# Performance work log

Measured on AMD Instinct MI355X. Metric: run time of the kernel, lower is better.

## Reference

```python
import jax, jax.numpy as jnp
import numpy as np

T = 262144        # sequence_length
K = 512           # num_basis
DEGREE = 3
EPS = 1e-6


def setup_inputs() -> dict:
    # Deterministic buffers, matching the torch module's __init__ exactly.
    t = jnp.linspace(-1.0, 1.0, T, dtype=jnp.float32)
    num_knots = K + DEGREE + 1
    inner = jnp.linspace(-1.0, 1.0, num_knots - 2 * DEGREE, dtype=jnp.float32)
    knots = jnp.concatenate([
        jnp.full((DEGREE,), -1.0, dtype=jnp.float32),
        inner,
        jnp.full((DEGREE,), 1.0, dtype=jnp.float32),
    ])
    return {"t": t, "knots": knots}


def _bspline(t, kv):
    n0 = K + DEGREE  # number of degree-0 basis functions
    tc = t[:, None]  # [T, 1]
    # degree-0: indicator of [kv[i], kv[i+1]) ; last interval is closed.
    cond1 = tc >= kv[None, :n0]
    cond2 = tc < kv[None, 1:n0 + 1]
    last_closed = tc <= kv[None, n0:n0 + 1]
    cond2 = jnp.concatenate([cond2[:, :-1], last_closed], axis=1)
    bases = (cond1 & cond2).astype(t.dtype)  # [T, K+DEGREE]
    # Cox-de Boor recursion, vectorized over knot index i.
    for d in range(1, DEGREE + 1):
        n = K + DEGREE - d
        den1 = kv[d:d + n] - kv[:n]            # [n]
        den2 = kv[d + 1:d + n + 1] - kv[1:n + 1]
        c1 = jnp.where(den1 >= EPS, (tc - kv[None, :n]) / jnp.where(den1 >= EPS, den1, 1.0), 0.0)
        c2 = jnp.where(den2 >= EPS, (kv[None, d + 1:d + n + 1] - tc) / jnp.where(den2 >= EPS, den2, 1.0), 0.0)
        bases = c1 * bases[:, :n] + c2 * bases[:, 1:n + 1]
    return bases  # [T, K]


def reference(t, knots):
    return _bspline(t, knots)
```

## Files before the change

### kernel.cpp

```cpp
#include <hip/hip_runtime.h>


namespace {
constexpr int K_N  = 512;
constexpr int NKN  = 516;
constexpr int DEG  = 3;
constexpr float EPSF = 1e-6f;
constexpr int ROWS = 16;
constexpr int BLK  = 256;
}

__global__ __launch_bounds__(BLK)
void bspline_basis_kernel(const float* __restrict__ t_arr,
                          const float* __restrict__ knots,
                          float* __restrict__ out)
{
    __shared__ float kv[NKN];

    const int tid = threadIdx.x;
    for (int i = tid; i < NKN; i += BLK) kv[i] = knots[i];

    const int row_base = blockIdx.x * ROWS;
    float4* out4 = reinterpret_cast<float4*>(out + (size_t)row_base * K_N);

    __syncthreads();

    int   j0 = -1;
    float N0 = 0.f, N1 = 0.f, N2 = 0.f, N3 = 0.f;
    if (tid < ROWS) {
        const float t = t_arr[row_base + tid];
        if (t < kv[K_N]) {
            int lo = DEG, hi = K_N - 1;
            while (lo < hi) {
                const int mid = (lo + hi + 1) >> 1;
                if (t >= kv[mid]) lo = mid; else hi = mid - 1;
            }
            const int s = lo;
            float N[4] = {1.f, 0.f, 0.f, 0.f};
            #pragma unroll
            for (int d = 1; d <= DEG; ++d) {
                float nn[4];
                #pragma unroll
                for (int k = 0; k <= d; ++k) {
                    const int j = s - d + k;
                    const float left  = (k >= 1)     ? N[k - 1] : 0.f;
                    const float right = (k <= d - 1) ? N[k]     : 0.f;
                    const float den1 = kv[j + d]     - kv[j];
                    const float den2 = kv[j + d + 1] - kv[j + 1];
                    const float c1 = (den1 >= EPSF) ? (t - kv[j]) / den1 : 0.f;
                    const float c2 = (den2 >= EPSF) ? (kv[j + d + 1] - t) / den2 : 0.f;
                    nn[k] = c1 * left + c2 * right;
                }
                #pragma unroll
                for (int k = 0; k <= d; ++k) N[k] = nn[k];
            }
            j0 = s - DEG;
            N0 = N[0]; N1 = N[1]; N2 = N[2]; N3 = N[3];
        }
    }

    const float4 z = make_float4(0.f, 0.f, 0.f, 0.f);
    constexpr int TOTAL_F4 = ROWS * (K_N / 4);
    #pragma unroll
    for (int it = 0; it < TOTAL_F4 / BLK; ++it)
        out4[it * BLK + tid] = z;

    __syncthreads();

    if (tid < ROWS && j0 >= 0) {
        float* p = out + (size_t)(row_base + tid) * K_N + j0;
        p[0] = N0; p[1] = N1; p[2] = N2; p[3] = N3;
    }
}

extern "C" void kernel_launch(void* const* d_in, const int* in_sizes, int n_in,
                              void* d_out, int out_size, void* d_ws, size_t ws_size,
                              hipStream_t stream) {
    const float* t_arr = (const float*)d_in[0];
    const float* knots = (const float*)d_in[1];
    float* out = (float*)d_out;
    const int n_rows = in_sizes[0];
    dim3 grid(n_rows / ROWS);
    hipLaunchKernelGGL(bspline_basis_kernel, grid, dim3(BLK), 0, stream,
                       t_arr, knots, out);
}
```

Measured before the change: 538.7 us.

## Split into grid-stride zero-fill kernel and window-write kernel with eight lanes per row

Splits the work into a grid-stride zero-fill kernel over the whole output and a second kernel where eight lanes per row each compute the basis and write float4 chunks covering the nonzero window. Moving the zeroing out of the per-row blocks is meant to make the dominant 512 MB write a dense streaming store. The cost is rewriting the window region a second time from another launch, plus eight-fold redundant binary search and recursion per row.

```diff
diff --git a/kernel.cpp b/kernel.cpp
--- a/kernel.cpp
+++ b/kernel.cpp
@@ -6,70 +6,87 @@
 constexpr int NKN  = 516;
 constexpr int DEG  = 3;
 constexpr float EPSF = 1e-6f;
-constexpr int ROWS = 16;
 constexpr int BLK  = 256;
+constexpr int ROWS_PER_BLK_B = 32;
 }
 
 __global__ __launch_bounds__(BLK)
-void bspline_basis_kernel(const float* __restrict__ t_arr,
-                          const float* __restrict__ knots,
-                          float* __restrict__ out)
+void zero_fill_kernel(float4* __restrict__ out4, int n4)
+{
+    const int stride = gridDim.x * BLK;
+    const float4 z = make_float4(0.f, 0.f, 0.f, 0.f);
+    for (int i = blockIdx.x * BLK + threadIdx.x; i < n4; i += stride)
+        out4[i] = z;
+}
+
+__global__ __launch_bounds__(BLK)
+void window_kernel(const float* __restrict__ t_arr,
+                   const float* __restrict__ knots,
+                   float* __restrict__ out)
 {
     __shared__ float kv[NKN];
-
     const int tid = threadIdx.x;
     for (int i = tid; i < NKN; i += BLK) kv[i] = knots[i];
-
-    const int row_base = blockIdx.x * ROWS;
-    float4* out4 = reinterpret_cast<float4*>(out + (size_t)row_base * K_N);
-
     __syncthreads();
 
-    int   j0 = -1;
-    float N0 = 0.f, N1 = 0.f, N2 = 0.f, N3 = 0.f;
-    if (tid < ROWS) {
-        const float t = t_arr[row_base + tid];
-        if (t < kv[K_N]) {
-            int lo = DEG, hi = K_N - 1;
-            while (lo < hi) {
-                const int mid = (lo + hi + 1) >> 1;
-                if (t >= kv[mid]) lo = mid; else hi = mid - 1;
-            }
-            const int s = lo;
-            float N[4] = {1.f, 0.f, 0.f, 0.f};
-            #pragma unroll
-            for (int d = 1; d <= DEG; ++d) {
-                float nn[4];
-                #pragma unroll
-                for (int k = 0; k <= d; ++k) {
-                    const int j = s - d + k;
-                    const float left  = (k >= 1)     ? N[k - 1] : 0.f;
-                    const float right = (k <= d - 1) ? N[k]     : 0.f;
-                    const float den1 = kv[j + d]     - kv[j];
-                    const float den2 = kv[j + d + 1] - kv[j + 1];
-                    const float c1 = (den1 >= EPSF) ? (t - kv[j]) / den1 : 0.f;
-                    const float c2 = (den2 >= EPSF) ? (kv[j + d + 1] - t) / den2 : 0.f;
-                    nn[k] = c1 * left + c2 * right;
-                }
-                #pragma unroll
-                for (int k = 0; k <= d; ++k) N[k] = nn[k];
-            }
-            j0 = s - DEG;
-            N0 = N[0]; N1 = N[1]; N2 = N[2]; N3 = N[3];
+    const int q   = tid & 7;
+    const int row = blockIdx.x * ROWS_PER_BLK_B + (tid >> 3);
+    const float t = t_arr[row];
+
+    if (t >= kv[K_N]) return;
+
+    int lo = DEG, hi = K_N - 1;
+    while (lo < hi) {
+        const int mid = (lo + hi + 1) >> 1;
+        if (t >= kv[mid]) lo = mid; else hi = mid - 1;
+    }
+    const int s = lo;
+
+    float N[4] = {1.f, 0.f, 0.f, 0.f};
+    #pragma unroll
+    for (int d = 1; d <= DEG; ++d) {
+        float nn[4];
+        #pragma unroll
+        for (int k = 0; k <= d; ++k) {
+            const int j = s - d + k;
+            const float left  = (k >= 1)     ? N[k - 1] : 0.f;
+            const float right = (k <= d - 1) ? N[k]     : 0.f;
+            const float den1 = kv[j + d]     - kv[j];
+            const float den2 = kv[j + d + 1] - kv[j + 1];
+            const float c1 = (den1 >= EPSF) ? (t - kv[j]) / den1 : 0.f;
+            const float c2 = (den2 >= EPSF) ? (kv[j + d + 1] - t) / den2 : 0.f;
+            nn[k] = c1 * left + c2 * right;
         }
+        #pragma unroll
+        for (int k = 0; k <= d; ++k) N[k] = nn[k];
     }
+    const int j0 = s - DEG;
 
-    const float4 z = make_float4(0.f, 0.f, 0.f, 0.f);
-    constexpr int TOTAL_F4 = ROWS * (K_N / 4);
-    #pragma unroll
-    for (int it = 0; it < TOTAL_F4 / BLK; ++it)
-        out4[it * BLK + tid] = z;
+    float4* row4 = reinterpret_cast<float4*>(out + (size_t)row * K_N);
+    const int l0 = j0 >> 5;
+    const int l1 = (j0 + 3) >> 5;
 
-    __syncthreads();
-
-    if (tid < ROWS && j0 >= 0) {
-        float* p = out + (size_t)(row_base + tid) * K_N + j0;
-        p[0] = N0; p[1] = N1; p[2] = N2; p[3] = N3;
+    {
+        const int cbase = (l0 << 5) + (q << 2);
+        float e[4];
+        #pragma unroll
+        for (int k = 0; k < 4; ++k) {
+            const int rel = cbase + k - j0;
+            e[k] = (rel == 0) ? N[0] : (rel == 1) ? N[1]
+                 : (rel == 2) ? N[2] : (rel == 3) ? N[3] : 0.f;
+        }
+        row4[(l0 << 3) + q] = make_float4(e[0], e[1], e[2], e[3]);
+    }
+    if (l1 != l0) {
+        const int cbase = (l1 << 5) + (q << 2);
+        float e[4];
+        #pragma unroll
+        for (int k = 0; k < 4; ++k) {
+            const int rel = cbase + k - j0;
+            e[k] = (rel == 0) ? N[0] : (rel == 1) ? N[1]
+                 : (rel == 2) ? N[2] : (rel == 3) ? N[3] : 0.f;
+        }
+        row4[(l1 << 3) + q] = make_float4(e[0], e[1], e[2], e[3]);
     }
 }
 
@@ -80,7 +97,10 @@
     const float* knots = (const float*)d_in[1];
     float* out = (float*)d_out;
     const int n_rows = in_sizes[0];
-    dim3 grid(n_rows / ROWS);
-    hipLaunchKernelGGL(bspline_basis_kernel, grid, dim3(BLK), 0, stream,
+    const int n4 = (n_rows * K_N) / 4;
+
+    hipLaunchKernelGGL(zero_fill_kernel, dim3(2048), dim3(BLK), 0, stream,
+                       reinterpret_cast<float4*>(out), n4);
+    hipLaunchKernelGGL(window_kernel, dim3(n_rows / ROWS_PER_BLK_B), dim3(BLK), 0, stream,
                        t_arr, knots, out);
 }
```

Result: slower. 568.0 us (+5.4%).
